# Kernel tuning notes

Measured on AMD Instinct MI355X. Metric: run time of the kernel, lower is better.

Reference implementation:

```python
import jax, jax.numpy as jnp
import numpy as np

B, N, C, H, DEPTH = 64, 256, 384, 8, 6
HD = C // H  # 48
SCALE = HD ** -0.5
LN_EPS = 1e-5


def setup_inputs() -> dict:
    key = jax.random.key(0)
    ks = jax.random.split(key, 12)
    g = lambda k, shape, s=0.05: jax.random.normal(k, shape, jnp.float32) * s
    return {
        "x": jax.random.normal(ks[0], (B, N, 2), jnp.float32),
        "mask": jnp.zeros((B, N), jnp.float32),  # additive padding mask (0 = keep)
        "emb_w1": g(ks[1], (C, 2), 0.5),
        "emb_b1": jnp.zeros((C,), jnp.float32),
        "emb_w2": g(ks[2], (C, C)),
        "emb_b2": jnp.zeros((C,), jnp.float32),
        "qkv_w": g(ks[3], (DEPTH, 3 * C, C)),
        "proj_w": g(ks[4], (DEPTH, C, C)),
        "proj_b": jnp.zeros((DEPTH, C), jnp.float32),
        "mlp_w1": g(ks[5], (DEPTH, C, C)),
        "mlp_b1": jnp.zeros((DEPTH, C), jnp.float32),
        "mlp_w2": g(ks[6], (DEPTH, C, C)),
        "mlp_b2": jnp.zeros((DEPTH, C), jnp.float32),
        "ln1_s": jnp.ones((DEPTH, C), jnp.float32),
        "ln1_b": jnp.zeros((DEPTH, C), jnp.float32),
        "ln2_s": jnp.ones((DEPTH, C), jnp.float32),
        "ln2_b": jnp.zeros((DEPTH, C), jnp.float32),
    }


def _layernorm(x, s, b):
    mu = jnp.mean(x, axis=-1, keepdims=True)
    var = jnp.mean((x - mu) ** 2, axis=-1, keepdims=True)
    return (x - mu) * jax.lax.rsqrt(var + LN_EPS) * s + b


def _rope(t):
    # t: (B, H, N, HD); interleaved rotary, matching the torch module
    hd = t.shape[-1]
    inv_freq = 1.0 / (10000.0 ** (jnp.arange(0, hd, 2, dtype=jnp.float32) / hd))
    pos = jnp.arange(t.shape[2], dtype=jnp.float32)
    f = pos[:, None] * inv_freq[None, :]            # (N, HD/2)
    cos, sin = jnp.cos(f), jnp.sin(f)
    xu, xe = t[..., 0::2], t[..., 1::2]
    ru = xu * cos - xe * sin
    re = xu * sin + xe * cos
    return jnp.stack([ru, re], axis=-1).reshape(t.shape)


def reference(x, mask, emb_w1, emb_b1, emb_w2, emb_b2, qkv_w, proj_w, proj_b,
              mlp_w1, mlp_b1, mlp_w2, mlp_b2, ln1_s, ln1_b, ln2_s, ln2_b):
    # BallEmbedding: Linear -> ReLU -> Linear
    h = jax.nn.relu(x @ emb_w1.T + emb_b1) @ emb_w2.T + emb_b2  # (B, N, C)
    for i in range(DEPTH):
        # pre-norm rotary attention
        y = _layernorm(h, ln1_s[i], ln1_b[i])
        qkv = (y @ qkv_w[i].T).reshape(B, N, 3, H, HD).transpose(2, 0, 3, 1, 4)
        q, k, v = qkv[0], qkv[1], qkv[2]                      # (B, H, N, HD)
        q = _rope(q) * SCALE
        k = _rope(k)
        attn = jnp.einsum('bhqd,bhkd->bhqk', q, k)
        attn = attn + mask[:, None, None, :] + mask[:, None, :, None]
        attn = jax.nn.softmax(attn, axis=-1)
        o = jnp.einsum('bhqk,bhkd->bhqd', attn, v)
        o = o.transpose(0, 2, 1, 3).reshape(B, N, C)
        h = h + (o @ proj_w[i].T + proj_b[i])
        # pre-norm MLP (hidden = dim, ReLU)
        y = _layernorm(h, ln2_s[i], ln2_b[i])
        m = jax.nn.relu(y @ mlp_w1[i].T + mlp_b1[i]) @ mlp_w2[i].T + mlp_b2[i]
        h = h + m
    return h
```

## Files before the change

kernel.cpp:

```cpp
#include <hip/hip_runtime.h>
#include <hip/hip_bf16.h>
#include <math.h>

#define BATCH 64
#define SEQ   256
#define CH    384
#define NHEAD 8
#define HD    48
#define DEPTH 6
#define NTOK  (BATCH*SEQ)
#define C3    (3*CH)
#define LN_EPS 1e-5f
#define ATT_SCALE 0.14433756729740643f

typedef __attribute__((ext_vector_type(8)))  short bf16x8;
typedef __attribute__((ext_vector_type(4)))  float f32x4;
typedef __attribute__((ext_vector_type(16))) float f32x16;

__device__ __forceinline__ ushort f2bf(float f) {
    __hip_bfloat16 h = __float2bfloat16(f);
    return *(ushort*)&h;
}
__device__ __forceinline__ float bfu2f(ushort u) {
    uint t = ((uint)u) << 16;
    union { uint u; float f; } c; c.u = t; return c.f;
}
__device__ __forceinline__ uint pk2(float a, float b) {
    return (uint)f2bf(a) | ((uint)f2bf(b) << 16);
}

#define AS1(p) ((const __attribute__((address_space(1))) void*)(p))
#define AS3(p) ((__attribute__((address_space(3))) void*)(uintptr_t)(p))
#define WAITVMC(N) asm volatile("s_waitcnt vmcnt(" #N ")" ::: "memory")
#define TAILSYNC() do { \
    asm volatile("s_waitcnt lgkmcnt(0)" ::: "memory"); \
    __builtin_amdgcn_sched_barrier(0); \
    __builtin_amdgcn_s_barrier(); } while (0)

__global__ void f2bf4_kernel(const float* __restrict__ in, ushort* __restrict__ out) {
    int i = (blockIdx.x*256 + threadIdx.x)*4;
    float4 v = *(const float4*)(in + i);
    ushort4 o;
    o.x = f2bf(v.x); o.y = f2bf(v.y); o.z = f2bf(v.z); o.w = f2bf(v.w);
    *(ushort4*)(out + i) = o;
}

__global__ void rope_table_kernel(float2* __restrict__ tbl) {
    int pos = threadIdx.x;
    for (int j = 0; j < 24; ++j) {
        float freq = exp2f(-(float)j * (13.287712379549449f / 24.0f));
        float ang = (float)pos * freq;
        float s, c;
        sincosf(ang, &s, &c);
        tbl[pos*24 + j] = make_float2(c, s);
    }
}

__global__ void embed1_kernel(const float* __restrict__ x, const float* __restrict__ w1,
                              const float* __restrict__ b1, ushort* __restrict__ out) {
    int idx = blockIdx.x*256 + threadIdx.x;
    int m = idx / CH, c = idx - m*CH;
    float v = x[m*2]*w1[c*2] + x[m*2+1]*w1[c*2+1] + b1[c];
    out[idx] = f2bf(fmaxf(v, 0.f));
}

__global__ __launch_bounds__(256) void prep_kernel(
        const float* __restrict__ Wsrc, const float* __restrict__ gam,
        const float* __restrict__ bet, const float* __restrict__ bias,
        int npl, ushort* __restrict__ Wdst, float2* __restrict__ uvout) {
    int rr   = blockIdx.x*4 + (threadIdx.x >> 6);
    int lane = threadIdx.x & 63;
    int layer = rr / npl;
    const float* wp = Wsrc + (size_t)rr*CH;
    const float* gp = gam + layer*CH;
    const float* bp = bet + layer*CH;
    float u = 0.f, vv = 0.f;
    if (lane < 48) {
        int c0 = lane*8;
        float w8[8];
        *(float4*)&w8[0] = *(const float4*)(wp + c0);
        *(float4*)&w8[4] = *(const float4*)(wp + c0 + 4);
        union { ushort us[8]; bf16x8 v; } o;
        #pragma unroll
        for (int j = 0; j < 8; ++j) {
            float wg = w8[j] * gp[c0+j];
            u  += wg;
            vv += bp[c0+j] * w8[j];
            o.us[j] = f2bf(wg);
        }
        *(bf16x8*)(Wdst + (size_t)rr*CH + c0) = o.v;
    }
    #pragma unroll
    for (int o = 1; o < 64; o <<= 1) { u += __shfl_xor(u, o); vv += __shfl_xor(vv, o); }
    if (lane == 0) {
        if (bias) vv += bias[rr];
        uvout[rr] = make_float2(u, vv);
    }
}

__global__ __launch_bounds__(256) void stats_kernel(const ushort* __restrict__ hbf,
                                                    float2* __restrict__ rstat) {
    int row  = blockIdx.x*4 + (threadIdx.x >> 6);
    int lane = threadIdx.x & 63;
    float v[8];
    float s = 0.f;
    bool act = lane < 48;
    if (act) {
        union { ushort us[8]; bf16x8 v; } x;
        x.v = *(const bf16x8*)(hbf + (size_t)row*CH + lane*8);
        #pragma unroll
        for (int j = 0; j < 8; ++j) { v[j] = bfu2f(x.us[j]); s += v[j]; }
    }
    #pragma unroll
    for (int o = 1; o < 64; o <<= 1) s += __shfl_xor(s, o);
    float mu = s * (1.0f/CH);
    float q = 0.f;
    if (act) {
        #pragma unroll
        for (int j = 0; j < 8; ++j) { float d = v[j]-mu; q += d*d; }
    }
    #pragma unroll
    for (int o = 1; o < 64; o <<= 1) q += __shfl_xor(q, o);
    if (lane == 0) rstat[row] = make_float2(mu, rsqrtf(q*(1.0f/CH) + LN_EPS));
}

template<bool LNAFF, bool RELU, bool RESID>
__global__ __launch_bounds__(256) void gemm_kernel(
        const ushort* __restrict__ A,
        const ushort* __restrict__ W,
        const float*  __restrict__ bias,
        const float2* __restrict__ uv,
        const float2* __restrict__ rstat,
        const float*  __restrict__ resid,
        float*  __restrict__ hout,
        ushort* __restrict__ bout,
        int ldo) {
    __shared__ __align__(16) ushort As[2][8192];
    __shared__ __align__(16) ushort Bs[2][8192];
    const int tid  = threadIdx.x;
    const int lane = tid & 63;
    const int w    = tid >> 6;
    const int l15  = lane & 15;
    const int g    = lane >> 4;
    const int wr   = (w >> 1) * 64;
    const int wc   = (w & 1) * 64;
    const int m0   = blockIdx.y * 128;
    const int n0   = blockIdx.x * 128;

    const int srow = lane >> 3;
    const int scol = ((lane & 7) ^ srow) * 8;
    auto stage = [&](int pb, int t) {
        int k0 = t*64;
        #pragma unroll
        for (int c = 0; c < 8; ++c) {
            int chunk = w + c*4;
            if (chunk < 16) {
                const ushort* gp = A + (size_t)(m0 + chunk*8 + srow)*CH + k0 + scol;
                __builtin_amdgcn_global_load_lds(AS1(gp), AS3(&As[pb][chunk*512]), 16, 0, 0);
            } else {
                const ushort* gp = W + (size_t)(n0 + (chunk-16)*8 + srow)*CH + k0 + scol;
                __builtin_amdgcn_global_load_lds(AS1(gp), AS3(&Bs[pb][(chunk-16)*512]), 16, 0, 0);
            }
        }
    };

    f32x4 acc[4][4] = {};
    const int xm = (l15 & 7) << 4;

    stage(0, 0);
    for (int t = 0; t < 6; ++t) {
        if (t + 1 < 6) stage((t+1)&1, t+1);
        if (t < 5) { WAITVMC(8); } else { WAITVMC(0); }
        __builtin_amdgcn_s_barrier();
        const int pb = t & 1;
        #pragma unroll
        for (int kk = 0; kk < 2; ++kk) {
            bf16x8 a[4], b[4];
            #pragma unroll
            for (int i = 0; i < 4; ++i)
                a[i] = *(const bf16x8*)((const char*)As[pb]
                        + (wr + i*16 + l15)*128 + ((kk*64 + 16*g) ^ xm));
            #pragma unroll
            for (int j = 0; j < 4; ++j)
                b[j] = *(const bf16x8*)((const char*)Bs[pb]
                        + (wc + j*16 + l15)*128 + ((kk*64 + 16*g) ^ xm));
            #pragma unroll
            for (int i = 0; i < 4; ++i)
                #pragma unroll
                for (int j = 0; j < 4; ++j)
                    acc[i][j] = __builtin_amdgcn_mfma_f32_16x16x32_bf16(a[i], b[j], acc[i][j], 0, 0, 0);
        }
        TAILSYNC();
    }

    const int cbase = n0 + wc + l15;
    const int rbase = m0 + wr + g*4;
    if (LNAFF) {
        float2 uvv[4];
        #pragma unroll
        for (int j = 0; j < 4; ++j) uvv[j] = uv[cbase + j*16];
        #pragma unroll
        for (int i = 0; i < 4; ++i)
            #pragma unroll
            for (int r = 0; r < 4; ++r) {
                int m = rbase + i*16 + r;
                float2 st = rstat[m];
                #pragma unroll
                for (int j = 0; j < 4; ++j) {
                    float v = st.y*(acc[i][j][r] - st.x*uvv[j].x) + uvv[j].y;
                    if (RELU) v = fmaxf(v, 0.f);
                    bout[(size_t)m*ldo + cbase + j*16] = f2bf(v);
                }
            }
    } else {
        float bj[4];
        #pragma unroll
        for (int j = 0; j < 4; ++j) bj[j] = bias[cbase + j*16];
        #pragma unroll
        for (int i = 0; i < 4; ++i)
            #pragma unroll
            for (int r = 0; r < 4; ++r) {
                int m = rbase + i*16 + r;
                #pragma unroll
                for (int j = 0; j < 4; ++j) {
                    int n = cbase + j*16;
                    float v = acc[i][j][r] + bj[j];
                    if (RESID) v += resid[(size_t)m*CH + n];
                    hout[(size_t)m*CH + n] = v;
                    bout[(size_t)m*CH + n] = f2bf(v);
                }
            }
    }
}

__global__ __launch_bounds__(512) void attn_kernel(
        const ushort* __restrict__ qkv, const float* __restrict__ mask,
        const float2* __restrict__ tbl, ushort* __restrict__ obuf) {
    __shared__ __align__(16) ushort Kf[8*3*64*8];
    __shared__ __align__(16) ushort Vf[2*16*64*8];
    __shared__ float Ms[SEQ];

    const int bid = blockIdx.x;
    const int b   = bid >> 3;
    const int hh  = bid & 7;
    const int tid = threadIdx.x;
    const int lane = tid & 63;
    const int hi   = (lane >> 5);
    const int q5   = lane & 31;
    const ushort* base = qkv + (size_t)b*SEQ*C3;

    {
        int t   = tid >> 6;
        int row = t*32 + q5;
        const ushort* kp = base + (size_t)row*C3 + CH + hh*HD;
        #pragma unroll
        for (int s = 0; s < 3; ++s) {
            union { ushort us[8]; bf16x8 v; } raw;
            raw.v = *(const bf16x8*)(kp + s*16 + hi*8);
            union { uint w[4]; bf16x8 v; } u;
            #pragma unroll
            for (int p = 0; p < 4; ++p) {
                float2 cs = tbl[row*24 + s*8 + hi*4 + p];
                float xu = bfu2f(raw.us[2*p]), xe = bfu2f(raw.us[2*p+1]);
                u.w[p] = pk2(xu*cs.x - xe*cs.y, xu*cs.y + xe*cs.x);
            }
            *(bf16x8*)&Kf[((t*3 + s)*64 + lane)*8] = u.v;
        }
    }
    {
        #pragma unroll
        for (int p = 0; p < 4; ++p) {
            int dt = p >> 1;
            int sp = (tid >> 6)*2 + (p & 1);
            int dd = dt*32 + q5;
            union { uint w[4]; bf16x8 v; } u;
            if (dd < HD) {
                const ushort* vp = base + (size_t)(sp*16 + hi*8)*C3 + 2*CH + hh*HD + dd;
                #pragma unroll
                for (int k = 0; k < 4; ++k)
                    u.w[k] = (uint)vp[(2*k)*C3] | ((uint)vp[(2*k+1)*C3] << 16);
            } else {
                u.w[0] = u.w[1] = u.w[2] = u.w[3] = 0u;
            }
            *(bf16x8*)&Vf[((dt*16 + sp)*64 + lane)*8] = u.v;
        }
    }
    if (tid < SEQ) Ms[tid] = mask[b*SEQ + tid];

    const int wv    = tid >> 6;
    const int qrow  = wv*32 + q5;
    bf16x8 qf[3];
    {
        const ushort* qp = base + (size_t)qrow*C3 + hh*HD;
        #pragma unroll
        for (int s = 0; s < 3; ++s) {
            union { ushort us[8]; bf16x8 v; } raw;
            raw.v = *(const bf16x8*)(qp + s*16 + hi*8);
            union { uint w[4]; bf16x8 v; } u;
            #pragma unroll
            for (int p = 0; p < 4; ++p) {
                float2 cs = tbl[qrow*24 + s*8 + hi*4 + p];
                float xu = bfu2f(raw.us[2*p]), xe = bfu2f(raw.us[2*p+1]);
                u.w[p] = pk2((xu*cs.x - xe*cs.y)*ATT_SCALE, (xu*cs.y + xe*cs.x)*ATT_SCALE);
            }
            qf[s] = u.v;
        }
    }
    __syncthreads();

    f32x16 st[8] = {};
    #pragma unroll
    for (int t = 0; t < 8; ++t)
        #pragma unroll
        for (int s = 0; s < 3; ++s) {
            bf16x8 af = *(const bf16x8*)&Kf[((t*3 + s)*64 + lane)*8];
            st[t] = __builtin_amdgcn_mfma_f32_32x32x16_bf16(af, qf[s], st[t], 0, 0, 0);
        }

    float mx = -1e30f;
    #pragma unroll
    for (int t = 0; t < 8; ++t)
        #pragma unroll
        for (int r = 0; r < 16; ++r) {
            int kt = t*32 + (r & 3) + 8*(r >> 2) + 4*hi;
            float s = st[t][r] + Ms[kt];
            st[t][r] = s;
            mx = fmaxf(mx, s);
        }
    mx = fmaxf(mx, __shfl_xor(mx, 32));
    float sum = 0.f;
    #pragma unroll
    for (int t = 0; t < 8; ++t)
        #pragma unroll
        for (int r = 0; r < 16; ++r) {
            float p = __expf(st[t][r] - mx);
            st[t][r] = p;
            sum += p;
        }
    sum += __shfl_xor(sum, 32);

    f32x16 oacc[2] = {};
    #pragma unroll
    for (int t = 0; t < 8; ++t) {
        uint w[4][2];
        #pragma unroll
        for (int g = 0; g < 4; ++g) {
            w[g][0] = pk2(st[t][g*4+0], st[t][g*4+1]);
            w[g][1] = pk2(st[t][g*4+2], st[t][g*4+3]);
        }
        #pragma unroll
        for (int o = 0; o < 2; ++o) {
            uint x0 = __shfl_xor(hi ? w[2*o][0] : w[2*o+1][0], 32);
            uint x1 = __shfl_xor(hi ? w[2*o][1] : w[2*o+1][1], 32);
            union { uint w[4]; bf16x8 v; } pf;
            if (hi == 0) { pf.w[0] = w[2*o][0]; pf.w[1] = w[2*o][1]; pf.w[2] = x0; pf.w[3] = x1; }
            else         { pf.w[0] = x0; pf.w[1] = x1; pf.w[2] = w[2*o+1][0]; pf.w[3] = w[2*o+1][1]; }
            int sp = t*2 + o;
            #pragma unroll
            for (int dt = 0; dt < 2; ++dt) {
                bf16x8 vf = *(const bf16x8*)&Vf[((dt*16 + sp)*64 + lane)*8];
                oacc[dt] = __builtin_amdgcn_mfma_f32_32x32x16_bf16(vf, pf.v, oacc[dt], 0, 0, 0);
            }
        }
    }

    float inv = 1.f / sum;
    ushort* op = obuf + ((size_t)(b*SEQ + qrow))*CH + hh*HD;
    #pragma unroll
    for (int dt = 0; dt < 2; ++dt)
        #pragma unroll
        for (int rg = 0; rg < 4; ++rg) {
            int d0 = dt*32 + rg*8 + hi*4;
            if (d0 < HD) {
                uint2 val;
                val.x = pk2(oacc[dt][rg*4+0]*inv, oacc[dt][rg*4+1]*inv);
                val.y = pk2(oacc[dt][rg*4+2]*inv, oacc[dt][rg*4+3]*inv);
                *(uint2*)(op + d0) = val;
            }
        }
}

extern "C" void kernel_launch(void* const* d_in, const int* in_sizes, int n_in,
                              void* d_out, int out_size, void* d_ws, size_t ws_size,
                              hipStream_t stream) {
    const float* x      = (const float*)d_in[0];
    const float* mask   = (const float*)d_in[1];
    const float* emb_w1 = (const float*)d_in[2];
    const float* emb_b1 = (const float*)d_in[3];
    const float* emb_w2 = (const float*)d_in[4];
    const float* emb_b2 = (const float*)d_in[5];
    const float* qkv_w  = (const float*)d_in[6];
    const float* proj_w = (const float*)d_in[7];
    const float* proj_b = (const float*)d_in[8];
    const float* mlp_w1 = (const float*)d_in[9];
    const float* mlp_b1 = (const float*)d_in[10];
    const float* mlp_w2 = (const float*)d_in[11];
    const float* mlp_b2 = (const float*)d_in[12];
    const float* ln1_s  = (const float*)d_in[13];
    const float* ln1_b  = (const float*)d_in[14];
    const float* ln2_s  = (const float*)d_in[15];
    const float* ln2_b  = (const float*)d_in[16];

    const size_t S1 = (size_t)NTOK*CH;
    float*  h     = (float*)d_ws;
    ushort* hbf   = (ushort*)(h + S1);
    ushort* qkvbf = hbf + S1;
    ushort* ybf   = qkvbf + 3*S1;
    ushort* t2bf  = ybf  + S1;
    ushort* obf   = t2bf + S1;
    ushort* wb_emb2 = obf + S1;
    ushort* wb_proj = wb_emb2 + 147456;
    ushort* wb_m2   = wb_proj + 884736;
    ushort* wqkvp   = wb_m2   + 884736;
    ushort* wm1p    = wqkvp   + 2654208;
    float2* uv_qkv  = (float2*)(wm1p + 884736);
    float2* uv_m1   = uv_qkv + 6912;
    float2* rstat   = uv_m1  + 2304;
    float*  tbl     = (float*)(rstat + 16384);

    dim3 gqkv(9, 128);
    dim3 g384(3, 128);

    rope_table_kernel<<<1, 256, 0, stream>>>((float2*)tbl);
    f2bf4_kernel<<<144, 256, 0, stream>>>(emb_w2, wb_emb2);
    f2bf4_kernel<<<864, 256, 0, stream>>>(proj_w, wb_proj);
    f2bf4_kernel<<<864, 256, 0, stream>>>(mlp_w2, wb_m2);
    prep_kernel<<<1728, 256, 0, stream>>>(qkv_w,  ln1_s, ln1_b, nullptr, C3, wqkvp, uv_qkv);
    prep_kernel<<<576,  256, 0, stream>>>(mlp_w1, ln2_s, ln2_b, mlp_b1,  CH, wm1p,  uv_m1);

    embed1_kernel<<<(NTOK*CH)/256, 256, 0, stream>>>(x, emb_w1, emb_b1, ybf);
    gemm_kernel<false,false,false><<<g384, 256, 0, stream>>>(ybf, wb_emb2, emb_b2,
            nullptr, nullptr, nullptr, h, hbf, CH);
    stats_kernel<<<NTOK/4, 256, 0, stream>>>(hbf, rstat);

    for (int i = 0; i < DEPTH; ++i) {
        gemm_kernel<true,false,false><<<gqkv, 256, 0, stream>>>(hbf,
                wqkvp + (size_t)i*C3*CH, nullptr, uv_qkv + i*C3, rstat,
                nullptr, nullptr, qkvbf, C3);
        attn_kernel<<<BATCH*NHEAD, 512, 0, stream>>>(qkvbf, mask, (const float2*)tbl, obf);
        gemm_kernel<false,false,true><<<g384, 256, 0, stream>>>(obf,
                wb_proj + (size_t)i*CH*CH, proj_b + i*CH, nullptr, nullptr,
                h, h, hbf, CH);
        stats_kernel<<<NTOK/4, 256, 0, stream>>>(hbf, rstat);
        gemm_kernel<true,true,false><<<g384, 256, 0, stream>>>(hbf,
                wm1p + (size_t)i*CH*CH, nullptr, uv_m1 + i*CH, rstat,
                nullptr, nullptr, t2bf, CH);
        gemm_kernel<false,false,true><<<g384, 256, 0, stream>>>(t2bf,
                wb_m2 + (size_t)i*CH*CH, mlp_b2 + i*CH, nullptr, nullptr,
                h, h, hbf, CH);
        if (i < DEPTH-1) stats_kernel<<<NTOK/4, 256, 0, stream>>>(hbf, rstat);
    }
    hipMemcpyAsync(d_out, h, S1*sizeof(float), hipMemcpyDeviceToDevice, stream);
}
```

Baseline: 836.8 us.

## Fuse layernorm stats into GEMM epilogues and write transposed V from QKV GEMM

Removes the separate stats kernels. The residual-writing GEMM epilogues now accumulate per-row sum and sum-of-squares into a zeroed buffer with atomics, and consumers derive mean and rstd from those sums. The QKV GEMM also writes V in a head-major transposed layout, so attention loads contiguous vectors instead of doing strided scalar gathers. This adds atomic traffic, uses a less numerically stable E[x^2]-mu^2 variance, and adds an extra zeroing kernel and buffer.

```diff
diff --git a/kernel.cpp b/kernel.cpp
--- a/kernel.cpp
+++ b/kernel.cpp
@@ -36,6 +36,10 @@
     asm volatile("s_waitcnt lgkmcnt(0)" ::: "memory"); \
     __builtin_amdgcn_sched_barrier(0); \
     __builtin_amdgcn_s_barrier(); } while (0)
+
+__global__ void zero_kernel(float4* __restrict__ p) {
+    p[blockIdx.x*256 + threadIdx.x] = float4{0.f,0.f,0.f,0.f};
+}
 
 __global__ void f2bf4_kernel(const float* __restrict__ in, ushort* __restrict__ out) {
     int i = (blockIdx.x*256 + threadIdx.x)*4;
@@ -98,43 +102,19 @@
     }
 }
 
-__global__ __launch_bounds__(256) void stats_kernel(const ushort* __restrict__ hbf,
-                                                    float2* __restrict__ rstat) {
-    int row  = blockIdx.x*4 + (threadIdx.x >> 6);
-    int lane = threadIdx.x & 63;
-    float v[8];
-    float s = 0.f;
-    bool act = lane < 48;
-    if (act) {
-        union { ushort us[8]; bf16x8 v; } x;
-        x.v = *(const bf16x8*)(hbf + (size_t)row*CH + lane*8);
-        #pragma unroll
-        for (int j = 0; j < 8; ++j) { v[j] = bfu2f(x.us[j]); s += v[j]; }
-    }
-    #pragma unroll
-    for (int o = 1; o < 64; o <<= 1) s += __shfl_xor(s, o);
-    float mu = s * (1.0f/CH);
-    float q = 0.f;
-    if (act) {
-        #pragma unroll
-        for (int j = 0; j < 8; ++j) { float d = v[j]-mu; q += d*d; }
-    }
-    #pragma unroll
-    for (int o = 1; o < 64; o <<= 1) q += __shfl_xor(q, o);
-    if (lane == 0) rstat[row] = make_float2(mu, rsqrtf(q*(1.0f/CH) + LN_EPS));
-}
-
-template<bool LNAFF, bool RELU, bool RESID>
+template<bool LNAFF, bool RELU, bool RESID, bool QKV>
 __global__ __launch_bounds__(256) void gemm_kernel(
         const ushort* __restrict__ A,
         const ushort* __restrict__ W,
         const float*  __restrict__ bias,
         const float2* __restrict__ uv,
-        const float2* __restrict__ rstat,
+        const float2* __restrict__ sbr,
         const float*  __restrict__ resid,
         float*  __restrict__ hout,
         ushort* __restrict__ bout,
-        int ldo) {
+        int ldo,
+        float2* __restrict__ sbw,
+        ushort* __restrict__ vtbuf) {
     __shared__ __align__(16) ushort As[2][8192];
     __shared__ __align__(16) ushort Bs[2][8192];
     const int tid  = threadIdx.x;
@@ -199,19 +179,52 @@
         float2 uvv[4];
         #pragma unroll
         for (int j = 0; j < 4; ++j) uvv[j] = uv[cbase + j*16];
-        #pragma unroll
-        for (int i = 0; i < 4; ++i)
+        const bool isV = QKV && (n0 >= 2*CH);
+        int hj[4], dj[4];
+        if (isV) {
+            #pragma unroll
+            for (int j = 0; j < 4; ++j) {
+                int nn = cbase + j*16 - 2*CH;
+                hj[j] = nn / HD; dj[j] = nn - hj[j]*HD;
+            }
+        }
+        #pragma unroll
+        for (int i = 0; i < 4; ++i) {
+            float muv[4], invv[4];
             #pragma unroll
             for (int r = 0; r < 4; ++r) {
-                int m = rbase + i*16 + r;
-                float2 st = rstat[m];
+                float2 s2 = sbr[rbase + i*16 + r];
+                float mu = s2.x * (1.0f/CH);
+                float var = s2.y * (1.0f/CH) - mu*mu;
+                muv[r] = mu; invv[r] = rsqrtf(var + LN_EPS);
+            }
+            if (isV) {
+                int bb   = rbase >> 8;
+                int seq0 = (rbase + i*16) & 255;
                 #pragma unroll
                 for (int j = 0; j < 4; ++j) {
-                    float v = st.y*(acc[i][j][r] - st.x*uvv[j].x) + uvv[j].y;
-                    if (RELU) v = fmaxf(v, 0.f);
-                    bout[(size_t)m*ldo + cbase + j*16] = f2bf(v);
+                    float vr[4];
+                    #pragma unroll
+                    for (int r = 0; r < 4; ++r)
+                        vr[r] = invv[r]*(acc[i][j][r] - muv[r]*uvv[j].x) + uvv[j].y;
+                    uint2 val;
+                    val.x = pk2(vr[0], vr[1]);
+                    val.y = pk2(vr[2], vr[3]);
+                    *(uint2*)(vtbuf + (((size_t)bb*NHEAD + hj[j])*HD + dj[j])*SEQ + seq0) = val;
                 }
-            }
+            } else {
+                #pragma unroll
+                for (int r = 0; r < 4; ++r) {
+                    int m = rbase + i*16 + r;
+                    #pragma unroll
+                    for (int j = 0; j < 4; ++j) {
+                        float v = invv[r]*(acc[i][j][r] - muv[r]*uvv[j].x) + uvv[j].y;
+                        if (RELU) v = fmaxf(v, 0.f);
+                        bout[(size_t)m*ldo + cbase + j*16] = f2bf(v);
+                    }
+                }
+            }
+        }
     } else {
         float bj[4];
         #pragma unroll
@@ -226,15 +239,40 @@
                     int n = cbase + j*16;
                     float v = acc[i][j][r] + bj[j];
                     if (RESID) v += resid[(size_t)m*CH + n];
+                    acc[i][j][r] = v;
                     hout[(size_t)m*CH + n] = v;
                     bout[(size_t)m*CH + n] = f2bf(v);
                 }
             }
+        if (sbw) {
+            #pragma unroll
+            for (int i = 0; i < 4; ++i)
+                #pragma unroll
+                for (int r = 0; r < 4; ++r) {
+                    float s = 0.f, q = 0.f;
+                    #pragma unroll
+                    for (int j = 0; j < 4; ++j) {
+                        float v = acc[i][j][r];
+                        s += v; q += v*v;
+                    }
+                    #pragma unroll
+                    for (int off = 1; off < 16; off <<= 1) {
+                        s += __shfl_xor(s, off);
+                        q += __shfl_xor(q, off);
+                    }
+                    if (l15 == 0) {
+                        int m = rbase + i*16 + r;
+                        atomicAdd(&sbw[m].x, s);
+                        atomicAdd(&sbw[m].y, q);
+                    }
+                }
+        }
     }
 }
 
 __global__ __launch_bounds__(512) void attn_kernel(
-        const ushort* __restrict__ qkv, const float* __restrict__ mask,
+        const ushort* __restrict__ qkv, const ushort* __restrict__ vtbuf,
+        const float* __restrict__ mask,
         const float2* __restrict__ tbl, ushort* __restrict__ obuf) {
     __shared__ __align__(16) ushort Kf[8*3*64*8];
     __shared__ __align__(16) ushort Vf[2*16*64*8];
@@ -268,21 +306,15 @@
         }
     }
     {
+        const ushort* vt = vtbuf + (size_t)(b*NHEAD + hh)*HD*SEQ;
         #pragma unroll
         for (int p = 0; p < 4; ++p) {
             int dt = p >> 1;
             int sp = (tid >> 6)*2 + (p & 1);
             int dd = dt*32 + q5;
-            union { uint w[4]; bf16x8 v; } u;
-            if (dd < HD) {
-                const ushort* vp = base + (size_t)(sp*16 + hi*8)*C3 + 2*CH + hh*HD + dd;
-                #pragma unroll
-                for (int k = 0; k < 4; ++k)
-                    u.w[k] = (uint)vp[(2*k)*C3] | ((uint)vp[(2*k+1)*C3] << 16);
-            } else {
-                u.w[0] = u.w[1] = u.w[2] = u.w[3] = 0u;
-            }
-            *(bf16x8*)&Vf[((dt*16 + sp)*64 + lane)*8] = u.v;
+            bf16x8 u = (bf16x8)(short)0;
+            if (dd < HD) u = *(const bf16x8*)(vt + (size_t)dd*SEQ + sp*16 + hi*8);
+            *(bf16x8*)&Vf[((dt*16 + sp)*64 + lane)*8] = u;
         }
     }
     if (tid < SEQ) Ms[tid] = mask[b*SEQ + tid];
@@ -408,19 +440,21 @@
     ushort* ybf   = qkvbf + 3*S1;
     ushort* t2bf  = ybf  + S1;
     ushort* obf   = t2bf + S1;
-    ushort* wb_emb2 = obf + S1;
+    ushort* vtbuf = obf  + S1;
+    ushort* wb_emb2 = vtbuf + S1;
     ushort* wb_proj = wb_emb2 + 147456;
     ushort* wb_m2   = wb_proj + 884736;
     ushort* wqkvp   = wb_m2   + 884736;
     ushort* wm1p    = wqkvp   + 2654208;
     float2* uv_qkv  = (float2*)(wm1p + 884736);
     float2* uv_m1   = uv_qkv + 6912;
-    float2* rstat   = uv_m1  + 2304;
-    float*  tbl     = (float*)(rstat + 16384);
+    float2* sb      = uv_m1  + 2304;
+    float*  tbl     = (float*)(sb + 12*NTOK);
 
     dim3 gqkv(9, 128);
     dim3 g384(3, 128);
 
+    zero_kernel<<<384, 256, 0, stream>>>((float4*)sb);
     rope_table_kernel<<<1, 256, 0, stream>>>((float2*)tbl);
     f2bf4_kernel<<<144, 256, 0, stream>>>(emb_w2, wb_emb2);
     f2bf4_kernel<<<864, 256, 0, stream>>>(proj_w, wb_proj);
@@ -429,26 +463,24 @@
     prep_kernel<<<576,  256, 0, stream>>>(mlp_w1, ln2_s, ln2_b, mlp_b1,  CH, wm1p,  uv_m1);
 
     embed1_kernel<<<(NTOK*CH)/256, 256, 0, stream>>>(x, emb_w1, emb_b1, ybf);
-    gemm_kernel<false,false,false><<<g384, 256, 0, stream>>>(ybf, wb_emb2, emb_b2,
-            nullptr, nullptr, nullptr, h, hbf, CH);
-    stats_kernel<<<NTOK/4, 256, 0, stream>>>(hbf, rstat);
+    gemm_kernel<false,false,false,false><<<g384, 256, 0, stream>>>(ybf, wb_emb2, emb_b2,
+            nullptr, nullptr, nullptr, h, hbf, CH, sb, nullptr);
 
     for (int i = 0; i < DEPTH; ++i) {
-        gemm_kernel<true,false,false><<<gqkv, 256, 0, stream>>>(hbf,
-                wqkvp + (size_t)i*C3*CH, nullptr, uv_qkv + i*C3, rstat,
-                nullptr, nullptr, qkvbf, C3);
-        attn_kernel<<<BATCH*NHEAD, 512, 0, stream>>>(qkvbf, mask, (const float2*)tbl, obf);
-        gemm_kernel<false,false,true><<<g384, 256, 0, stream>>>(obf,
+        gemm_kernel<true,false,false,true><<<gqkv, 256, 0, stream>>>(hbf,
+                wqkvp + (size_t)i*C3*CH, nullptr, uv_qkv + i*C3, sb + (size_t)(2*i)*NTOK,
+                nullptr, nullptr, qkvbf, C3, nullptr, vtbuf);
+        attn_kernel<<<BATCH*NHEAD, 512, 0, stream>>>(qkvbf, vtbuf, mask,
+                (const float2*)tbl, obf);
+        gemm_kernel<false,false,true,false><<<g384, 256, 0, stream>>>(obf,
                 wb_proj + (size_t)i*CH*CH, proj_b + i*CH, nullptr, nullptr,
-                h, h, hbf, CH);
-        stats_kernel<<<NTOK/4, 256, 0, stream>>>(hbf, rstat);
-        gemm_kernel<true,true,false><<<g384, 256, 0, stream>>>(hbf,
-                wm1p + (size_t)i*CH*CH, nullptr, uv_m1 + i*CH, rstat,
-                nullptr, nullptr, t2bf, CH);
-        gemm_kernel<false,false,true><<<g384, 256, 0, stream>>>(t2bf,
+                h, h, hbf, CH, sb + (size_t)(2*i+1)*NTOK, nullptr);
+        gemm_kernel<true,true,false,false><<<g384, 256, 0, stream>>>(hbf,
+                wm1p + (size_t)i*CH*CH, nullptr, uv_m1 + i*CH, sb + (size_t)(2*i+1)*NTOK,
+                nullptr, nullptr, t2bf, CH, nullptr, nullptr);
+        gemm_kernel<false,false,true,false><<<g384, 256, 0, stream>>>(t2bf,
                 wb_m2 + (size_t)i*CH*CH, mlp_b2 + i*CH, nullptr, nullptr,
-                h, h, hbf, CH);
-        if (i < DEPTH-1) stats_kernel<<<NTOK/4, 256, 0, stream>>>(hbf, rstat);
+                h, h, hbf, CH, (i < DEPTH-1) ? (sb + (size_t)(2*i+2)*NTOK) : nullptr, nullptr);
     }
     hipMemcpyAsync(d_out, h, S1*sizeof(float), hipMemcpyDeviceToDevice, stream);
 }
```

Result: slower. 856.1 us (+2.3%).
